# Optimization experiments

Measured on AMD Instinct MI355X. Metric: run time of the kernel, lower is better.

The kernel has to match this reference:

```python
import jax, jax.numpy as jnp
import numpy as np

N = 50000
E = 800000
IN_C, HID_C, OUT_C = 5, 64, 32


def setup_inputs() -> dict:
    key = jax.random.key(0)
    ks = jax.random.split(key, 9)
    x = jax.random.normal(ks[0], (N, IN_C), dtype=jnp.float32)
    edge_index = jax.random.randint(ks[1], (2, E), 0, N, dtype=jnp.int64)
    # SAGEConv params: lin_l (neighbor path, has bias), lin_r (root path, no bias)
    def lin(k, fan_out, fan_in):
        s = 1.0 / np.sqrt(fan_in)
        return jax.random.uniform(k, (fan_out, fan_in), jnp.float32, -s, s)
    W1l = lin(ks[2], HID_C, IN_C); b1 = jnp.zeros((HID_C,), jnp.float32); W1r = lin(ks[3], HID_C, IN_C)
    W2l = lin(ks[4], HID_C, HID_C); b2 = jnp.zeros((HID_C,), jnp.float32); W2r = lin(ks[5], HID_C, HID_C)
    W3l = lin(ks[6], OUT_C, HID_C); b3 = jnp.zeros((OUT_C,), jnp.float32); W3r = lin(ks[7], OUT_C, HID_C)
    return {"x": x, "edge_index": edge_index,
            "W1l": W1l, "b1": b1, "W1r": W1r,
            "W2l": W2l, "b2": b2, "W2r": W2r,
            "W3l": W3l, "b3": b3, "W3r": W3r}


def _sage_conv(x, src, dst, inv_deg, Wl, bl, Wr):
    # PyG SAGEConv (aggr='mean'): out = lin_l(mean_j x_j) + lin_r(x)
    msg = x[src]                                          # [E, d_in] gather
    agg = jax.ops.segment_sum(msg, dst, num_segments=N)   # [N, d_in] scatter-add
    mean = agg * inv_deg                                  # mean aggregation
    return mean @ Wl.T + bl + x @ Wr.T


def reference(x, edge_index, W1l, b1, W1r, W2l, b2, W2r, W3l, b3, W3r):
    src, dst = edge_index[0], edge_index[1]
    deg = jax.ops.segment_sum(jnp.ones((E,), x.dtype), dst, num_segments=N)
    inv_deg = (1.0 / jnp.maximum(deg, 1.0))[:, None]      # [N, 1]
    h = jax.nn.relu(_sage_conv(x, src, dst, inv_deg, W1l, b1, W1r))
    # F.dropout(p=0.2, training=self.training): identity in eval mode
    h = jax.nn.relu(_sage_conv(h, src, dst, inv_deg, W2l, b2, W2r))
    out = _sage_conv(h, src, dst, inv_deg, W3l, b3, W3r)
    return out
```

## Files before the change

### kernel.cpp

```cpp
#include <hip/hip_runtime.h>
#include <hip/hip_fp16.h>


#define N_NODES 50000
#define N_EDGES 800000
#define IN_C 5
#define HID_C 64
#define OUT_C 32

#define NB 196
#define BWG 800
#define BCH (N_EDGES / BWG)
#define PAD 32
#define WPB 48
#define SLOT 64
#define NPAD (NB * 256)

typedef __attribute__((ext_vector_type(8))) short bf16x8;
typedef __attribute__((ext_vector_type(4))) float f32x4;

__device__ __forceinline__ unsigned short f2bf(float f) {
    unsigned u = __float_as_uint(f);
    return (unsigned short)((u + 0x7fffu + ((u >> 16) & 1u)) >> 16);
}
__device__ __forceinline__ float bf2f(unsigned short b) {
    return __uint_as_float(((unsigned)b) << 16);
}
__device__ __forceinline__ float2 unpk_h2(unsigned u) {
    __half2 h = *(__half2*)&u;
    return __half22float2(h);
}


__global__ __launch_bounds__(256) void k_bucketcnt(
    const int* __restrict__ ei, unsigned* __restrict__ pbuf,
    unsigned char* __restrict__ cnt,
    const float* __restrict__ W2l, const float* __restrict__ W2r,
    const float* __restrict__ W3l, const float* __restrict__ W3r,
    unsigned short* __restrict__ W2hi, unsigned short* __restrict__ W2lo,
    unsigned short* __restrict__ W3zhi, unsigned short* __restrict__ W3zlo) {
    if (blockIdx.x >= BWG) {
        const int t = (blockIdx.x - BWG) * 256 + threadIdx.x;
        const int stride = WPB * 256;
        for (int p = t; p < 64 * 128; p += stride) {
            int j = p >> 7, k = p & 127;
            float w = (k < 64) ? W2l[j * 64 + k] : W2r[j * 64 + (k - 64)];
            unsigned short h = f2bf(w);
            W2hi[p] = h;
            W2lo[p] = f2bf(w - bf2f(h));
        }
        for (int p = t; p < 64 * 64; p += stride) {
            int j = p >> 6, k = p & 63;
            float w = (j < 32) ? W3l[j * 64 + k] : W3r[(j - 32) * 64 + k];
            unsigned short h = f2bf(w);
            W3zhi[p] = h;
            W3zlo[p] = f2bf(w - bf2f(h));
        }
        return;
    }
    __shared__ int cur[NB];
    __shared__ unsigned lbuf[NB * PAD];
    const int t = threadIdx.x;
    const int c = blockIdx.x;
    const int c0 = c * BCH;

    if (t < NB) cur[t] = 0;
    __syncthreads();
    for (int i = t; i < BCH; i += 256) {
        int s = ei[c0 + i];
        int d = ei[N_EDGES + c0 + i];
        int b = d >> 8;
        int pos = atomicAdd(&cur[b], 1);
        if (pos < PAD) lbuf[b * PAD + pos] = ((unsigned)(d & 255) << 16) | (unsigned)s;
    }
    __syncthreads();
    unsigned* dst = pbuf + (size_t)c * (NB * PAD);
    for (int i = t; i < NB * PAD; i += 256) dst[i] = lbuf[i];
    if (t < NB) {
        int cc = cur[t];
        cnt[c * NB + t] = (unsigned char)(cc < PAD ? cc : PAD);
    }
}


__global__ __launch_bounds__(256) void k_bsort_l1(
    const unsigned* __restrict__ pbuf, const unsigned char* __restrict__ cnt,
    int* __restrict__ deg, unsigned short* __restrict__ slots,
    const float* __restrict__ x, const float* __restrict__ W1l,
    const float* __restrict__ b1, const float* __restrict__ W1r,
    __half* __restrict__ h1) {
    __shared__ unsigned short lslot[256 * SLOT];
    __shared__ int cnt2[256];
    __shared__ unsigned char lcnt[BWG];
    __shared__ float w1l[64 * IN_C];
    __shared__ float w1r[64 * IN_C];
    __shared__ float bb1[64];
    const int t = threadIdx.x;
    const int b = blockIdx.x;

    for (int i = t; i < 64 * IN_C; i += 256) {
        w1l[i] = W1l[i];
        w1r[i] = W1r[i];
    }
    if (t < 64) bb1[t] = b1[t];
    cnt2[t] = 0;
    for (int i = t; i < BWG; i += 256) lcnt[i] = cnt[i * NB + b];
    __syncthreads();

    for (int i = t; i < BWG * PAD; i += 256) {
        int c = i >> 5;
        int k = i & (PAD - 1);
        if (k < (int)lcnt[c]) {
            unsigned ev = pbuf[((size_t)c * NB + b) * PAD + k];
            int ld = ev >> 16;
            int pos = atomicAdd(&cnt2[ld], 1);
            if (pos < SLOT) lslot[ld * SLOT + pos] = (unsigned short)(ev & 0xFFFFu);
        }
    }
    __syncthreads();

    const int node = (b << 8) + t;
    int d = cnt2[t];
    if (d > SLOT) d = SLOT;
    if (node < N_NODES) deg[node] = d;

    {
        const uint4* ls4 = (const uint4*)lslot;
        uint4* gs4 = (uint4*)(slots + (size_t)(b << 8) * SLOT);
        for (int i = t; i < 256 * SLOT / 8; i += 256) gs4[i] = ls4[i];
    }

    if (node >= N_NODES) return;
    float mm[IN_C] = {0.f, 0.f, 0.f, 0.f, 0.f};
    for (int i = 0; i < d; ++i) {
        int j = lslot[t * SLOT + i];
        const float* xp = x + j * IN_C;
#pragma unroll
        for (int q = 0; q < IN_C; ++q) mm[q] += xp[q];
    }
    const float idg = 1.0f / (float)(d > 1 ? d : 1);
#pragma unroll
    for (int q = 0; q < IN_C; ++q) mm[q] *= idg;
    float rr[IN_C];
    const float* xr = x + (size_t)node * IN_C;
#pragma unroll
    for (int q = 0; q < IN_C; ++q) rr[q] = xr[q];

    uint4* hrow = (uint4*)(h1 + (size_t)node * HID_C);
#pragma unroll
    for (int ob = 0; ob < 8; ++ob) {
        float oc[8];
#pragma unroll
        for (int q = 0; q < 8; ++q) {
            const int o = ob * 8 + q;
            float acc = bb1[o];
#pragma unroll
            for (int i = 0; i < IN_C; ++i) {
                acc = fmaf(w1l[o * IN_C + i], mm[i], acc);
                acc = fmaf(w1r[o * IN_C + i], rr[i], acc);
            }
            oc[q] = fmaxf(acc, 0.f);
        }
        unsigned uu[4];
#pragma unroll
        for (int q = 0; q < 4; ++q) {
            __half2 hh = __floats2half2_rn(oc[2 * q], oc[2 * q + 1]);
            uu[q] = *reinterpret_cast<unsigned*>(&hh);
        }
        hrow[ob] = make_uint4(uu[0], uu[1], uu[2], uu[3]);
    }
}


__global__ __launch_bounds__(256) void k_fused2(
    const __half* __restrict__ h, const int* __restrict__ deg,
    const unsigned short* __restrict__ slots,
    const unsigned short* __restrict__ W2hi, const unsigned short* __restrict__ W2lo,
    const float* __restrict__ b2,
    const unsigned short* __restrict__ W3zhi, const unsigned short* __restrict__ W3zlo,
    const float* __restrict__ b3,
    __half* __restrict__ z3l, float* __restrict__ z3r) {
    constexpr int AP = 152;
    __shared__ __align__(16) unsigned short Ah[32][AP];
    __shared__ __align__(16) unsigned short Al[32][AP];
    const int t = threadIdx.x;
    const int lane = t & 63;
    const int w = t >> 6;
    const int ns = lane >> 3;
    const int cg = lane & 7;
    const int node0 = blockIdx.x * 32;
    const int m = w * 8 + ns;
    const int v = node0 + m;
    const bool valid = v < N_NODES;
    const uint4* h4 = (const uint4*)h;

    int dg = 0;
    float idg = 0.f;
    uint4 ur = make_uint4(0u, 0u, 0u, 0u);
    if (valid) {
        dg = deg[v];
        if (dg > SLOT) dg = SLOT;
        idg = 1.0f / (float)(dg > 1 ? dg : 1);
        ur = h4[v * 8 + cg];
    }

    const unsigned short* sp = slots + (size_t)(valid ? v : 0) * SLOT;
    const int last = (dg > 0) ? (dg - 1) : 0;
#define SIDX(K) (int)sp[(K) < last ? (K) : last]
    int j0 = SIDX(0), j1 = SIDX(1), j2 = SIDX(2), j3 = SIDX(3);
    int j4 = SIDX(4), j5 = SIDX(5), j6 = SIDX(6), j7 = SIDX(7);

    float s0 = 0.f, s1 = 0.f, s2 = 0.f, s3 = 0.f;
    float s4 = 0.f, s5 = 0.f, s6 = 0.f, s7 = 0.f;
    for (int k = 0; k < dg; k += 8) {
        uint4 u0 = h4[j0 * 8 + cg];
        uint4 u1 = h4[j1 * 8 + cg];
        uint4 u2 = h4[j2 * 8 + cg];
        uint4 u3 = h4[j3 * 8 + cg];
        uint4 u4 = h4[j4 * 8 + cg];
        uint4 u5 = h4[j5 * 8 + cg];
        uint4 u6 = h4[j6 * 8 + cg];
        uint4 u7 = h4[j7 * 8 + cg];
        float w1 = (k + 1 < dg) ? 1.f : 0.f;
        float w2 = (k + 2 < dg) ? 1.f : 0.f;
        float w3 = (k + 3 < dg) ? 1.f : 0.f;
        float w4 = (k + 4 < dg) ? 1.f : 0.f;
        float w5 = (k + 5 < dg) ? 1.f : 0.f;
        float w6 = (k + 6 < dg) ? 1.f : 0.f;
        float w7 = (k + 7 < dg) ? 1.f : 0.f;
        j0 = SIDX(k + 8);  j1 = SIDX(k + 9);  j2 = SIDX(k + 10); j3 = SIDX(k + 11);
        j4 = SIDX(k + 12); j5 = SIDX(k + 13); j6 = SIDX(k + 14); j7 = SIDX(k + 15);
        {
            float2 a = unpk_h2(u0.x), b = unpk_h2(u0.y);
            float2 c = unpk_h2(u0.z), d = unpk_h2(u0.w);
            s0 += a.x; s1 += a.y; s2 += b.x; s3 += b.y;
            s4 += c.x; s5 += c.y; s6 += d.x; s7 += d.y;
        }
#define ACCW(U, W)                                                     \
        {                                                              \
            float2 a = unpk_h2(U.x), b = unpk_h2(U.y);                 \
            float2 c = unpk_h2(U.z), d = unpk_h2(U.w);                 \
            s0 = fmaf(a.x, W, s0); s1 = fmaf(a.y, W, s1);              \
            s2 = fmaf(b.x, W, s2); s3 = fmaf(b.y, W, s3);              \
            s4 = fmaf(c.x, W, s4); s5 = fmaf(c.y, W, s5);              \
            s6 = fmaf(d.x, W, s6); s7 = fmaf(d.y, W, s7);              \
        }
        ACCW(u1, w1) ACCW(u2, w2) ACCW(u3, w3)
        ACCW(u4, w4) ACCW(u5, w5) ACCW(u6, w6) ACCW(u7, w7)
#undef ACCW
    }
#undef SIDX

    float m0 = s0 * idg, m1 = s1 * idg, m2 = s2 * idg, m3 = s3 * idg;
    float m4 = s4 * idg, m5 = s5 * idg, m6 = s6 * idg, m7 = s7 * idg;

    {
        unsigned short a0 = f2bf(m0), a1 = f2bf(m1), a2 = f2bf(m2), a3 = f2bf(m3);
        unsigned short a4 = f2bf(m4), a5 = f2bf(m5), a6 = f2bf(m6), a7 = f2bf(m7);
        uint4 hi, lo;
        hi.x = (unsigned)a0 | ((unsigned)a1 << 16);
        hi.y = (unsigned)a2 | ((unsigned)a3 << 16);
        hi.z = (unsigned)a4 | ((unsigned)a5 << 16);
        hi.w = (unsigned)a6 | ((unsigned)a7 << 16);
        lo.x = (unsigned)f2bf(m0 - bf2f(a0)) | ((unsigned)f2bf(m1 - bf2f(a1)) << 16);
        lo.y = (unsigned)f2bf(m2 - bf2f(a2)) | ((unsigned)f2bf(m3 - bf2f(a3)) << 16);
        lo.z = (unsigned)f2bf(m4 - bf2f(a4)) | ((unsigned)f2bf(m5 - bf2f(a5)) << 16);
        lo.w = (unsigned)f2bf(m6 - bf2f(a6)) | ((unsigned)f2bf(m7 - bf2f(a7)) << 16);
        *(uint4*)&Ah[m][cg * 8] = hi;
        *(uint4*)&Al[m][cg * 8] = lo;
    }
    {
        float2 p0 = unpk_h2(ur.x), p1 = unpk_h2(ur.y);
        float2 p2 = unpk_h2(ur.z), p3 = unpk_h2(ur.w);
        unsigned short a0 = f2bf(p0.x), a1 = f2bf(p0.y), a2 = f2bf(p1.x), a3 = f2bf(p1.y);
        unsigned short a4 = f2bf(p2.x), a5 = f2bf(p2.y), a6 = f2bf(p3.x), a7 = f2bf(p3.y);
        uint4 hi, lo;
        hi.x = (unsigned)a0 | ((unsigned)a1 << 16);
        hi.y = (unsigned)a2 | ((unsigned)a3 << 16);
        hi.z = (unsigned)a4 | ((unsigned)a5 << 16);
        hi.w = (unsigned)a6 | ((unsigned)a7 << 16);
        lo.x = (unsigned)f2bf(p0.x - bf2f(a0)) | ((unsigned)f2bf(p0.y - bf2f(a1)) << 16);
        lo.y = (unsigned)f2bf(p1.x - bf2f(a2)) | ((unsigned)f2bf(p1.y - bf2f(a3)) << 16);
        lo.z = (unsigned)f2bf(p2.x - bf2f(a4)) | ((unsigned)f2bf(p2.y - bf2f(a5)) << 16);
        lo.w = (unsigned)f2bf(p3.x - bf2f(a6)) | ((unsigned)f2bf(p3.y - bf2f(a7)) << 16);
        *(uint4*)&Ah[m][64 + cg * 8] = hi;
        *(uint4*)&Al[m][64 + cg * 8] = lo;
    }
    __syncthreads();

    const int r = lane & 15;
    const int quad = lane >> 4;
    f32x4 accA = (f32x4){0.f, 0.f, 0.f, 0.f};
    f32x4 accB = (f32x4){0.f, 0.f, 0.f, 0.f};
#pragma unroll
    for (int ks = 0; ks < 4; ++ks) {
        bf16x8 ah0 = *(const bf16x8*)&Ah[r][ks * 32 + quad * 8];
        bf16x8 al0 = *(const bf16x8*)&Al[r][ks * 32 + quad * 8];
        bf16x8 ah1 = *(const bf16x8*)&Ah[16 + r][ks * 32 + quad * 8];
        bf16x8 al1 = *(const bf16x8*)&Al[16 + r][ks * 32 + quad * 8];
        const size_t wb = ((size_t)(w * 16 + r)) * 128 + ks * 32 + quad * 8;
        bf16x8 bh = *(const bf16x8*)(W2hi + wb);
        bf16x8 bl = *(const bf16x8*)(W2lo + wb);
        accA = __builtin_amdgcn_mfma_f32_16x16x32_bf16(ah0, bh, accA, 0, 0, 0);
        accA = __builtin_amdgcn_mfma_f32_16x16x32_bf16(ah0, bl, accA, 0, 0, 0);
        accA = __builtin_amdgcn_mfma_f32_16x16x32_bf16(al0, bh, accA, 0, 0, 0);
        accB = __builtin_amdgcn_mfma_f32_16x16x32_bf16(ah1, bh, accB, 0, 0, 0);
        accB = __builtin_amdgcn_mfma_f32_16x16x32_bf16(ah1, bl, accB, 0, 0, 0);
        accB = __builtin_amdgcn_mfma_f32_16x16x32_bf16(al1, bh, accB, 0, 0, 0);
    }
    const float bv2 = b2[w * 16 + r];
    float h2A[4], h2B[4];
#pragma unroll
    for (int g = 0; g < 4; ++g) {
        h2A[g] = fmaxf(accA[g] + bv2, 0.f);
        h2B[g] = fmaxf(accB[g] + bv2, 0.f);
    }
    __syncthreads();

#pragma unroll
    for (int g = 0; g < 4; ++g) {
        unsigned short hiA = f2bf(h2A[g]);
        Ah[quad * 4 + g][w * 16 + r] = hiA;
        Al[quad * 4 + g][w * 16 + r] = f2bf(h2A[g] - bf2f(hiA));
        unsigned short hiB = f2bf(h2B[g]);
        Ah[16 + quad * 4 + g][w * 16 + r] = hiB;
        Al[16 + quad * 4 + g][w * 16 + r] = f2bf(h2B[g] - bf2f(hiB));
    }
    __syncthreads();

    f32x4 zA = (f32x4){0.f, 0.f, 0.f, 0.f};
    f32x4 zB = (f32x4){0.f, 0.f, 0.f, 0.f};
#pragma unroll
    for (int ks = 0; ks < 2; ++ks) {
        bf16x8 ah0 = *(const bf16x8*)&Ah[r][ks * 32 + quad * 8];
        bf16x8 al0 = *(const bf16x8*)&Al[r][ks * 32 + quad * 8];
        bf16x8 ah1 = *(const bf16x8*)&Ah[16 + r][ks * 32 + quad * 8];
        bf16x8 al1 = *(const bf16x8*)&Al[16 + r][ks * 32 + quad * 8];
        const size_t wb = ((size_t)(w * 16 + r)) * 64 + ks * 32 + quad * 8;
        bf16x8 bh = *(const bf16x8*)(W3zhi + wb);
        bf16x8 bl = *(const bf16x8*)(W3zlo + wb);
        zA = __builtin_amdgcn_mfma_f32_16x16x32_bf16(ah0, bh, zA, 0, 0, 0);
        zA = __builtin_amdgcn_mfma_f32_16x16x32_bf16(ah0, bl, zA, 0, 0, 0);
        zA = __builtin_amdgcn_mfma_f32_16x16x32_bf16(al0, bh, zA, 0, 0, 0);
        zB = __builtin_amdgcn_mfma_f32_16x16x32_bf16(ah1, bh, zB, 0, 0, 0);
        zB = __builtin_amdgcn_mfma_f32_16x16x32_bf16(ah1, bl, zB, 0, 0, 0);
        zB = __builtin_amdgcn_mfma_f32_16x16x32_bf16(al1, bh, zB, 0, 0, 0);
    }
    const int j = w * 16 + r;
    const float badd = (j >= 32) ? b3[j - 32] : 0.f;
#pragma unroll
    for (int g = 0; g < 4; ++g) {
        int nodeA = node0 + quad * 4 + g;
        int nodeB = node0 + 16 + quad * 4 + g;
        float vA = zA[g] + badd;
        float vB = zB[g] + badd;
        if (nodeA < N_NODES) {
            if (j < 32) z3l[(size_t)nodeA * 32 + j] = __float2half(vA);
            else        z3r[(size_t)nodeA * 32 + (j - 32)] = vA;
        }
        if (nodeB < N_NODES) {
            if (j < 32) z3l[(size_t)nodeB * 32 + j] = __float2half(vB);
            else        z3r[(size_t)nodeB * 32 + (j - 32)] = vB;
        }
    }
}


__global__ __launch_bounds__(256) void k_agg3(
    const int* __restrict__ deg, const unsigned short* __restrict__ slots,
    const __half* __restrict__ z3l, const float* __restrict__ z3r,
    float* __restrict__ out) {
    const int t = threadIdx.x;
    const int lane = t & 63;
    const int v = blockIdx.x * 4 + (t >> 6);
    if (v >= N_NODES) return;
    const int slot = lane >> 2;
    const int cg = lane & 3;

    int d = deg[v];
    if (d > SLOT) d = SLOT;
    const float idg = 1.0f / (float)(d > 1 ? d : 1);
    const unsigned short* sp = slots + (size_t)v * SLOT;
    const uint4* z4 = (const uint4*)z3l;

    float s0 = 0.f, s1 = 0.f, s2 = 0.f, s3 = 0.f;
    float s4 = 0.f, s5 = 0.f, s6 = 0.f, s7 = 0.f;
    for (int k = 0; k < d; k += 16) {
        int o = k + slot;
        int oc = (o < d) ? o : (d - 1);
        if (oc < 0) oc = 0;
        int jn = sp[oc];
        uint4 u = z4[jn * 4 + cg];
        float wk = (o < d) ? 1.f : 0.f;
        float2 a = unpk_h2(u.x), b = unpk_h2(u.y);
        float2 c = unpk_h2(u.z), dd = unpk_h2(u.w);
        s0 = fmaf(a.x, wk, s0); s1 = fmaf(a.y, wk, s1);
        s2 = fmaf(b.x, wk, s2); s3 = fmaf(b.y, wk, s3);
        s4 = fmaf(c.x, wk, s4); s5 = fmaf(c.y, wk, s5);
        s6 = fmaf(dd.x, wk, s6); s7 = fmaf(dd.y, wk, s7);
    }
#pragma unroll
    for (int off = 4; off <= 32; off <<= 1) {
        s0 += __shfl_xor(s0, off, 64); s1 += __shfl_xor(s1, off, 64);
        s2 += __shfl_xor(s2, off, 64); s3 += __shfl_xor(s3, off, 64);
        s4 += __shfl_xor(s4, off, 64); s5 += __shfl_xor(s5, off, 64);
        s6 += __shfl_xor(s6, off, 64); s7 += __shfl_xor(s7, off, 64);
    }
    if (lane < 4) {
        const float4* zr4 = (const float4*)(z3r + (size_t)v * 32);
        float4 r0 = zr4[lane * 2];
        float4 r1 = zr4[lane * 2 + 1];
        float4 o0, o1;
        o0.x = fmaf(s0, idg, r0.x); o0.y = fmaf(s1, idg, r0.y);
        o0.z = fmaf(s2, idg, r0.z); o0.w = fmaf(s3, idg, r0.w);
        o1.x = fmaf(s4, idg, r1.x); o1.y = fmaf(s5, idg, r1.y);
        o1.z = fmaf(s6, idg, r1.z); o1.w = fmaf(s7, idg, r1.w);
        float4* op = (float4*)(out + (size_t)v * 32);
        op[lane * 2] = o0;
        op[lane * 2 + 1] = o1;
    }
}


extern "C" void kernel_launch(void* const* d_in, const int* in_sizes, int n_in,
                              void* d_out, int out_size, void* d_ws, size_t ws_size,
                              hipStream_t stream) {
    const float* x   = (const float*)d_in[0];
    const int*   ei  = (const int*)d_in[1];
    const float* W1l = (const float*)d_in[2];
    const float* b1  = (const float*)d_in[3];
    const float* W1r = (const float*)d_in[4];
    const float* W2l = (const float*)d_in[5];
    const float* b2  = (const float*)d_in[6];
    const float* W2r = (const float*)d_in[7];
    const float* W3l = (const float*)d_in[8];
    const float* b3  = (const float*)d_in[9];
    const float* W3r = (const float*)d_in[10];

    char* ws = (char*)d_ws;
    size_t off = 0;
    auto alloc = [&](size_t bytes) -> char* {
        char* p = ws + off;
        off += (bytes + 255) & ~(size_t)255;
        return p;
    };
    int*            deg   = (int*)alloc(N_NODES * sizeof(int));
    unsigned short* slots = (unsigned short*)alloc((size_t)NPAD * SLOT * sizeof(unsigned short));
    unsigned*       pbuf  = (unsigned*)alloc((size_t)BWG * NB * PAD * sizeof(unsigned));
    unsigned char*  cnt   = (unsigned char*)alloc((size_t)BWG * NB);
    __half*         h1    = (__half*)alloc((size_t)N_NODES * HID_C * sizeof(__half));
    __half*         z3l   = (__half*)alloc((size_t)N_NODES * OUT_C * sizeof(__half));
    float*          z3r   = (float*)alloc((size_t)N_NODES * OUT_C * sizeof(float));
    unsigned short* W2hi  = (unsigned short*)alloc(64 * 128 * 2);
    unsigned short* W2lo  = (unsigned short*)alloc(64 * 128 * 2);
    unsigned short* W3zhi = (unsigned short*)alloc(64 * 64 * 2);
    unsigned short* W3zlo = (unsigned short*)alloc(64 * 64 * 2);

    k_bucketcnt<<<dim3(BWG + WPB), dim3(256), 0, stream>>>(
        ei, pbuf, cnt, W2l, W2r, W3l, W3r, W2hi, W2lo, W3zhi, W3zlo);

    k_bsort_l1<<<dim3(NB), dim3(256), 0, stream>>>(
        pbuf, cnt, deg, slots, x, W1l, b1, W1r, h1);

    const int FT = (N_NODES + 31) / 32;
    k_fused2<<<dim3(FT), dim3(256), 0, stream>>>(
        h1, deg, slots, W2hi, W2lo, b2, W3zhi, W3zlo, b3, z3l, z3r);

    k_agg3<<<dim3((N_NODES + 3) / 4), dim3(256), 0, stream>>>(
        deg, slots, z3l, z3r, (float*)d_out);
}
```

Before: 185.2 us.

## Replace padded per-chunk bucket buffers with compacted global buckets and split sort

The edge bucketing pass now builds a local histogram, prefix-scans it, reserves space per bucket with a global atomic counter, and writes edges contiguously into a fixed-capacity per-bucket array instead of into padded per-chunk slots. The sort/layer-1 kernel then reads only the real edges of its bucket and launches four blocks per bucket, each handling 64 nodes, with the 64 output channels split across thread groups. This removes the scan over 800x32 mostly-empty padded entries and raises the block count. The cost is a memset, extra scan synchronisation, and each of the four blocks rereading the whole bucket while keeping only a quarter of it. Edge order within slots becomes nondeterministic.

```diff
diff --git a/kernel.cpp b/kernel.cpp
--- a/kernel.cpp
+++ b/kernel.cpp
@@ -9,9 +9,9 @@
 #define OUT_C 32
 
 #define NB 196
+#define BCAP 6144
 #define BWG 800
 #define BCH (N_EDGES / BWG)
-#define PAD 32
 #define WPB 48
 #define SLOT 64
 #define NPAD (NB * 256)
@@ -32,9 +32,9 @@
 }
 
 
-__global__ __launch_bounds__(256) void k_bucketcnt(
-    const int* __restrict__ ei, unsigned* __restrict__ pbuf,
-    unsigned char* __restrict__ cnt,
+__global__ __launch_bounds__(256) void k_bucketprep(
+    const int* __restrict__ ei, int* __restrict__ gcur,
+    unsigned* __restrict__ ebuf,
     const float* __restrict__ W2l, const float* __restrict__ W2r,
     const float* __restrict__ W3l, const float* __restrict__ W3r,
     unsigned short* __restrict__ W2hi, unsigned short* __restrict__ W2lo,
@@ -58,116 +58,148 @@
         }
         return;
     }
+    __shared__ int hist[NB];
+    __shared__ int loff[NB];
     __shared__ int cur[NB];
-    __shared__ unsigned lbuf[NB * PAD];
+    __shared__ int gbase[NB];
+    __shared__ int scanb[256];
+    __shared__ unsigned ev0[BCH];
+    __shared__ unsigned stage[BCH];
     const int t = threadIdx.x;
-    const int c = blockIdx.x;
-    const int c0 = c * BCH;
-
-    if (t < NB) cur[t] = 0;
+    const int c0 = blockIdx.x * BCH;
+
+    if (t < NB) hist[t] = 0;
     __syncthreads();
     for (int i = t; i < BCH; i += 256) {
         int s = ei[c0 + i];
         int d = ei[N_EDGES + c0 + i];
-        int b = d >> 8;
-        int pos = atomicAdd(&cur[b], 1);
-        if (pos < PAD) lbuf[b * PAD + pos] = ((unsigned)(d & 255) << 16) | (unsigned)s;
-    }
-    __syncthreads();
-    unsigned* dst = pbuf + (size_t)c * (NB * PAD);
-    for (int i = t; i < NB * PAD; i += 256) dst[i] = lbuf[i];
+        ev0[i] = ((unsigned)d << 16) | (unsigned)s;
+        atomicAdd(&hist[d >> 8], 1);
+    }
+    __syncthreads();
+    scanb[t] = (t < NB) ? hist[t] : 0;
+    __syncthreads();
+#pragma unroll
+    for (int o = 1; o < 256; o <<= 1) {
+        int v = scanb[t];
+        int a = (t >= o) ? scanb[t - o] : 0;
+        __syncthreads();
+        scanb[t] = v + a;
+        __syncthreads();
+    }
     if (t < NB) {
-        int cc = cur[t];
-        cnt[c * NB + t] = (unsigned char)(cc < PAD ? cc : PAD);
+        int ex = (t == 0) ? 0 : scanb[t - 1];
+        loff[t] = ex;
+        cur[t] = ex;
+        gbase[t] = atomicAdd(&gcur[t], hist[t]);
+    }
+    __syncthreads();
+    for (int i = t; i < BCH; i += 256) {
+        unsigned ev = ev0[i];
+        int b = ev >> 24;
+        int p = atomicAdd(&cur[b], 1);
+        stage[p] = ev;
+    }
+    __syncthreads();
+    for (int i = t; i < BCH; i += 256) {
+        unsigned ev = stage[i];
+        int b = ev >> 24;
+        int pos = gbase[b] + (i - loff[b]);
+        if (pos < BCAP) ebuf[b * BCAP + pos] = ev;
     }
 }
 
 
 __global__ __launch_bounds__(256) void k_bsort_l1(
-    const unsigned* __restrict__ pbuf, const unsigned char* __restrict__ cnt,
+    const int* __restrict__ gcur, const unsigned* __restrict__ ebuf,
     int* __restrict__ deg, unsigned short* __restrict__ slots,
     const float* __restrict__ x, const float* __restrict__ W1l,
     const float* __restrict__ b1, const float* __restrict__ W1r,
     __half* __restrict__ h1) {
-    __shared__ unsigned short lslot[256 * SLOT];
-    __shared__ int cnt2[256];
-    __shared__ unsigned char lcnt[BWG];
+    __shared__ unsigned short lslot[64 * SLOT];
+    __shared__ int cnt2[64];
     __shared__ float w1l[64 * IN_C];
     __shared__ float w1r[64 * IN_C];
     __shared__ float bb1[64];
     const int t = threadIdx.x;
-    const int b = blockIdx.x;
+    const int b = blockIdx.x >> 2;
+    const int q = blockIdx.x & 3;
 
     for (int i = t; i < 64 * IN_C; i += 256) {
         w1l[i] = W1l[i];
         w1r[i] = W1r[i];
     }
-    if (t < 64) bb1[t] = b1[t];
-    cnt2[t] = 0;
-    for (int i = t; i < BWG; i += 256) lcnt[i] = cnt[i * NB + b];
-    __syncthreads();
-
-    for (int i = t; i < BWG * PAD; i += 256) {
-        int c = i >> 5;
-        int k = i & (PAD - 1);
-        if (k < (int)lcnt[c]) {
-            unsigned ev = pbuf[((size_t)c * NB + b) * PAD + k];
-            int ld = ev >> 16;
-            int pos = atomicAdd(&cnt2[ld], 1);
-            if (pos < SLOT) lslot[ld * SLOT + pos] = (unsigned short)(ev & 0xFFFFu);
-        }
-    }
-    __syncthreads();
-
-    const int node = (b << 8) + t;
-    int d = cnt2[t];
+    if (t < 64) {
+        bb1[t] = b1[t];
+        cnt2[t] = 0;
+    }
+    __syncthreads();
+
+    int n = gcur[b];
+    if (n > BCAP) n = BCAP;
+    const unsigned* eb = ebuf + (size_t)b * BCAP;
+    for (int i = t; i < n; i += 256) {
+        unsigned ev = eb[i];
+        int ld = (ev >> 16) & 255;
+        if ((ld >> 6) == q) {
+            int pos = atomicAdd(&cnt2[ld & 63], 1);
+            if (pos < SLOT) lslot[(ld & 63) * SLOT + pos] = (unsigned short)(ev & 0xFFFFu);
+        }
+    }
+    __syncthreads();
+
+    const int node0 = (b << 8) + (q << 6);
+    const int ln = t & 63;
+    const int node = node0 + ln;
+    int d = cnt2[ln];
     if (d > SLOT) d = SLOT;
-    if (node < N_NODES) deg[node] = d;
+    if (t < 64 && node < N_NODES) deg[node] = d;
 
     {
         const uint4* ls4 = (const uint4*)lslot;
-        uint4* gs4 = (uint4*)(slots + (size_t)(b << 8) * SLOT);
-        for (int i = t; i < 256 * SLOT / 8; i += 256) gs4[i] = ls4[i];
+        uint4* gs4 = (uint4*)(slots + (size_t)node0 * SLOT);
+        for (int i = t; i < 512; i += 256) gs4[i] = ls4[i];
     }
 
     if (node >= N_NODES) return;
+    const int co = t >> 6;
     float mm[IN_C] = {0.f, 0.f, 0.f, 0.f, 0.f};
     for (int i = 0; i < d; ++i) {
-        int j = lslot[t * SLOT + i];
+        int j = lslot[ln * SLOT + i];
         const float* xp = x + j * IN_C;
 #pragma unroll
-        for (int q = 0; q < IN_C; ++q) mm[q] += xp[q];
+        for (int qq = 0; qq < IN_C; ++qq) mm[qq] += xp[qq];
     }
     const float idg = 1.0f / (float)(d > 1 ? d : 1);
 #pragma unroll
-    for (int q = 0; q < IN_C; ++q) mm[q] *= idg;
+    for (int qq = 0; qq < IN_C; ++qq) mm[qq] *= idg;
     float rr[IN_C];
     const float* xr = x + (size_t)node * IN_C;
 #pragma unroll
-    for (int q = 0; q < IN_C; ++q) rr[q] = xr[q];
+    for (int qq = 0; qq < IN_C; ++qq) rr[qq] = xr[qq];
 
     uint4* hrow = (uint4*)(h1 + (size_t)node * HID_C);
 #pragma unroll
-    for (int ob = 0; ob < 8; ++ob) {
+    for (int ob = 0; ob < 2; ++ob) {
         float oc[8];
 #pragma unroll
-        for (int q = 0; q < 8; ++q) {
-            const int o = ob * 8 + q;
+        for (int qq = 0; qq < 8; ++qq) {
+            const int o = co * 16 + ob * 8 + qq;
             float acc = bb1[o];
 #pragma unroll
             for (int i = 0; i < IN_C; ++i) {
                 acc = fmaf(w1l[o * IN_C + i], mm[i], acc);
                 acc = fmaf(w1r[o * IN_C + i], rr[i], acc);
             }
-            oc[q] = fmaxf(acc, 0.f);
+            oc[qq] = fmaxf(acc, 0.f);
         }
         unsigned uu[4];
 #pragma unroll
-        for (int q = 0; q < 4; ++q) {
-            __half2 hh = __floats2half2_rn(oc[2 * q], oc[2 * q + 1]);
-            uu[q] = *reinterpret_cast<unsigned*>(&hh);
-        }
-        hrow[ob] = make_uint4(uu[0], uu[1], uu[2], uu[3]);
+        for (int qq = 0; qq < 4; ++qq) {
+            __half2 hh = __floats2half2_rn(oc[2 * qq], oc[2 * qq + 1]);
+            uu[qq] = *reinterpret_cast<unsigned*>(&hh);
+        }
+        hrow[co * 2 + ob] = make_uint4(uu[0], uu[1], uu[2], uu[3]);
     }
 }
 
@@ -444,10 +476,10 @@
         off += (bytes + 255) & ~(size_t)255;
         return p;
     };
+    int*            gcur  = (int*)alloc(NB * sizeof(int));
     int*            deg   = (int*)alloc(N_NODES * sizeof(int));
     unsigned short* slots = (unsigned short*)alloc((size_t)NPAD * SLOT * sizeof(unsigned short));
-    unsigned*       pbuf  = (unsigned*)alloc((size_t)BWG * NB * PAD * sizeof(unsigned));
-    unsigned char*  cnt   = (unsigned char*)alloc((size_t)BWG * NB);
+    unsigned*       ebuf  = (unsigned*)alloc((size_t)NB * BCAP * sizeof(unsigned));
     __half*         h1    = (__half*)alloc((size_t)N_NODES * HID_C * sizeof(__half));
     __half*         z3l   = (__half*)alloc((size_t)N_NODES * OUT_C * sizeof(__half));
     float*          z3r   = (float*)alloc((size_t)N_NODES * OUT_C * sizeof(float));
@@ -456,11 +488,13 @@
     unsigned short* W3zhi = (unsigned short*)alloc(64 * 64 * 2);
     unsigned short* W3zlo = (unsigned short*)alloc(64 * 64 * 2);
 
-    k_bucketcnt<<<dim3(BWG + WPB), dim3(256), 0, stream>>>(
-        ei, pbuf, cnt, W2l, W2r, W3l, W3r, W2hi, W2lo, W3zhi, W3zlo);
-
-    k_bsort_l1<<<dim3(NB), dim3(256), 0, stream>>>(
-        pbuf, cnt, deg, slots, x, W1l, b1, W1r, h1);
+    hipMemsetAsync(gcur, 0, NB * sizeof(int), stream);
+
+    k_bucketprep<<<dim3(BWG + WPB), dim3(256), 0, stream>>>(
+        ei, gcur, ebuf, W2l, W2r, W3l, W3r, W2hi, W2lo, W3zhi, W3zlo);
+
+    k_bsort_l1<<<dim3(NB * 4), dim3(256), 0, stream>>>(
+        gcur, ebuf, deg, slots, x, W1l, b1, W1r, h1);
 
     const int FT = (N_NODES + 31) / 32;
     k_fused2<<<dim3(FT), dim3(256), 0, stream>>>(
```

Measured after the change: 174.4 us. 5.9% less time.

## Transpose partition buffers and split bucket sort across four blocks per bucket

Applied to the files above, without the earlier changes.

The partition buffer and count array are transposed to bucket-major order, so each bucket's entries from all edge chunks sit contiguously and the sort kernel reads them with coalesced loads. The slot-sort plus layer-1 kernel now launches four blocks per 256-node bucket. Each block handles 64 nodes, and its 256 threads each compute 16 of the 64 output channels. This raises parallelism from 196 blocks to 784. In exchange, each of the four blocks rescans the full bucket data and discards three quarters of it, and the partition kernel's writes become strided.

```diff
diff --git a/kernel.cpp b/kernel.cpp
--- a/kernel.cpp
+++ b/kernel.cpp
@@ -32,7 +32,7 @@
 }
 
 
-__global__ __launch_bounds__(256) void k_bucketcnt(
+__global__ __launch_bounds__(256) void k_part(
     const int* __restrict__ ei, unsigned* __restrict__ pbuf,
     unsigned char* __restrict__ cnt,
     const float* __restrict__ W2l, const float* __restrict__ W2r,
@@ -74,100 +74,112 @@
         if (pos < PAD) lbuf[b * PAD + pos] = ((unsigned)(d & 255) << 16) | (unsigned)s;
     }
     __syncthreads();
-    unsigned* dst = pbuf + (size_t)c * (NB * PAD);
-    for (int i = t; i < NB * PAD; i += 256) dst[i] = lbuf[i];
+    for (int i = t; i < NB * PAD; i += 256) {
+        int b = i >> 5;
+        int k = i & (PAD - 1);
+        pbuf[((size_t)b * BWG + c) * PAD + k] = lbuf[i];
+    }
     if (t < NB) {
         int cc = cur[t];
-        cnt[c * NB + t] = (unsigned char)(cc < PAD ? cc : PAD);
-    }
-}
-
-
-__global__ __launch_bounds__(256) void k_bsort_l1(
+        cnt[(size_t)t * BWG + c] = (unsigned char)(cc < PAD ? cc : PAD);
+    }
+}
+
+
+__global__ __launch_bounds__(256) void k_slots_l1(
     const unsigned* __restrict__ pbuf, const unsigned char* __restrict__ cnt,
     int* __restrict__ deg, unsigned short* __restrict__ slots,
     const float* __restrict__ x, const float* __restrict__ W1l,
     const float* __restrict__ b1, const float* __restrict__ W1r,
     __half* __restrict__ h1) {
-    __shared__ unsigned short lslot[256 * SLOT];
-    __shared__ int cnt2[256];
+    __shared__ unsigned short lslot[64 * SLOT];
+    __shared__ int cnt2[64];
     __shared__ unsigned char lcnt[BWG];
     __shared__ float w1l[64 * IN_C];
     __shared__ float w1r[64 * IN_C];
     __shared__ float bb1[64];
     const int t = threadIdx.x;
-    const int b = blockIdx.x;
+    const int b = blockIdx.x >> 2;
+    const int q = blockIdx.x & 3;
 
     for (int i = t; i < 64 * IN_C; i += 256) {
         w1l[i] = W1l[i];
         w1r[i] = W1r[i];
     }
-    if (t < 64) bb1[t] = b1[t];
-    cnt2[t] = 0;
-    for (int i = t; i < BWG; i += 256) lcnt[i] = cnt[i * NB + b];
-    __syncthreads();
-
+    if (t < 64) {
+        bb1[t] = b1[t];
+        cnt2[t] = 0;
+    }
+    for (int i = t; i < BWG; i += 256) lcnt[i] = cnt[(size_t)b * BWG + i];
+    __syncthreads();
+
+    const unsigned* pb = pbuf + (size_t)b * BWG * PAD;
     for (int i = t; i < BWG * PAD; i += 256) {
         int c = i >> 5;
         int k = i & (PAD - 1);
         if (k < (int)lcnt[c]) {
-            unsigned ev = pbuf[((size_t)c * NB + b) * PAD + k];
-            int ld = ev >> 16;
-            int pos = atomicAdd(&cnt2[ld], 1);
-            if (pos < SLOT) lslot[ld * SLOT + pos] = (unsigned short)(ev & 0xFFFFu);
-        }
-    }
-    __syncthreads();
-
-    const int node = (b << 8) + t;
-    int d = cnt2[t];
+            unsigned ev = pb[i];
+            int ld = (ev >> 16) & 255;
+            if ((ld >> 6) == q) {
+                int pos = atomicAdd(&cnt2[ld & 63], 1);
+                if (pos < SLOT) lslot[(ld & 63) * SLOT + pos] = (unsigned short)(ev & 0xFFFFu);
+            }
+        }
+    }
+    __syncthreads();
+
+    const int node0 = (b << 8) + (q << 6);
+    const int ln = t & 63;
+    const int node = node0 + ln;
+    int d = cnt2[ln];
     if (d > SLOT) d = SLOT;
-    if (node < N_NODES) deg[node] = d;
+    if (t < 64 && node < N_NODES) deg[node] = d;
 
     {
         const uint4* ls4 = (const uint4*)lslot;
-        uint4* gs4 = (uint4*)(slots + (size_t)(b << 8) * SLOT);
-        for (int i = t; i < 256 * SLOT / 8; i += 256) gs4[i] = ls4[i];
+        uint4* gs4 = (uint4*)(slots + (size_t)node0 * SLOT);
+        for (int i = t; i < 512; i += 256) gs4[i] = ls4[i];
     }
 
     if (node >= N_NODES) return;
+    const int co = t >> 6;
     float mm[IN_C] = {0.f, 0.f, 0.f, 0.f, 0.f};
     for (int i = 0; i < d; ++i) {
-        int j = lslot[t * SLOT + i];
+        int j = lslot[ln * SLOT + i];
         const float* xp = x + j * IN_C;
 #pragma unroll
-        for (int q = 0; q < IN_C; ++q) mm[q] += xp[q];
+        for (int qq = 0; qq < IN_C; ++qq) mm[qq] += xp[qq];
     }
     const float idg = 1.0f / (float)(d > 1 ? d : 1);
 #pragma unroll
-    for (int q = 0; q < IN_C; ++q) mm[q] *= idg;
+    for (int qq = 0; qq < IN_C; ++qq) mm[qq] *= idg;
     float rr[IN_C];
     const float* xr = x + (size_t)node * IN_C;
 #pragma unroll
-    for (int q = 0; q < IN_C; ++q) rr[q] = xr[q];
+    for (int qq = 0; qq < IN_C; ++qq) rr[qq] = xr[qq];
 
     uint4* hrow = (uint4*)(h1 + (size_t)node * HID_C);
 #pragma unroll
-    for (int ob = 0; ob < 8; ++ob) {
+    for (int ob = 0; ob < 2; ++ob) {
         float oc[8];
 #pragma unroll
-        for (int q = 0; q < 8; ++q) {
-            const int o = ob * 8 + q;
+        for (int qq = 0; qq < 8; ++qq) {
+            const int o = co * 16 + ob * 8 + qq;
             float acc = bb1[o];
 #pragma unroll
             for (int i = 0; i < IN_C; ++i) {
                 acc = fmaf(w1l[o * IN_C + i], mm[i], acc);
                 acc = fmaf(w1r[o * IN_C + i], rr[i], acc);
             }
-            oc[q] = fmaxf(acc, 0.f);
+            oc[qq] = fmaxf(acc, 0.f);
         }
         unsigned uu[4];
 #pragma unroll
-        for (int q = 0; q < 4; ++q) {
-            __half2 hh = __floats2half2_rn(oc[2 * q], oc[2 * q + 1]);
-            uu[q] = *reinterpret_cast<unsigned*>(&hh);
-        }
-        hrow[ob] = make_uint4(uu[0], uu[1], uu[2], uu[3]);
+        for (int qq = 0; qq < 4; ++qq) {
+            __half2 hh = __floats2half2_rn(oc[2 * qq], oc[2 * qq + 1]);
+            uu[qq] = *reinterpret_cast<unsigned*>(&hh);
+        }
+        hrow[co * 2 + ob] = make_uint4(uu[0], uu[1], uu[2], uu[3]);
     }
 }
 
@@ -446,8 +458,8 @@
     };
     int*            deg   = (int*)alloc(N_NODES * sizeof(int));
     unsigned short* slots = (unsigned short*)alloc((size_t)NPAD * SLOT * sizeof(unsigned short));
-    unsigned*       pbuf  = (unsigned*)alloc((size_t)BWG * NB * PAD * sizeof(unsigned));
-    unsigned char*  cnt   = (unsigned char*)alloc((size_t)BWG * NB);
+    unsigned*       pbuf  = (unsigned*)alloc((size_t)NB * BWG * PAD * sizeof(unsigned));
+    unsigned char*  cnt   = (unsigned char*)alloc((size_t)NB * BWG);
     __half*         h1    = (__half*)alloc((size_t)N_NODES * HID_C * sizeof(__half));
     __half*         z3l   = (__half*)alloc((size_t)N_NODES * OUT_C * sizeof(__half));
     float*          z3r   = (float*)alloc((size_t)N_NODES * OUT_C * sizeof(float));
@@ -456,10 +468,10 @@
     unsigned short* W3zhi = (unsigned short*)alloc(64 * 64 * 2);
     unsigned short* W3zlo = (unsigned short*)alloc(64 * 64 * 2);
 
-    k_bucketcnt<<<dim3(BWG + WPB), dim3(256), 0, stream>>>(
+    k_part<<<dim3(BWG + WPB), dim3(256), 0, stream>>>(
         ei, pbuf, cnt, W2l, W2r, W3l, W3r, W2hi, W2lo, W3zhi, W3zlo);
 
-    k_bsort_l1<<<dim3(NB), dim3(256), 0, stream>>>(
+    k_slots_l1<<<dim3(NB * 4), dim3(256), 0, stream>>>(
         pbuf, cnt, deg, slots, x, W1l, b1, W1r, h1);
 
     const int FT = (N_NODES + 31) / 32;
```

After: 194.2 us. 1.05x slower.
